# Performance work log

Measured on AMD Instinct MI355X. Metric: run time of the kernel, lower is better.

Reference implementation:

```python
import jax, jax.numpy as jnp
import numpy as np

EPS = 1e-5      # BatchNorm1d default eps
K = 4           # branching factor of the ontology tree
HID = 6         # num_hiddens_genotype
LEVEL_SIZES = (64, 16, 4, 1)   # leaves -> root (term_layer_list order)
OFFSETS = (0, 64, 80, 84)      # slices into the stacked [85,...] term params


def setup_inputs() -> dict:
    key = jax.random.key(0)
    ks = jax.random.split(key, 8)
    B, G, GD, NT, NL = 4096, 4096, 24, 85, 64
    f32 = jnp.float32
    return {
        "x": jax.random.normal(ks[0], (B, G), f32),
        "gene_W": jax.random.normal(ks[1], (NL, GD, G), f32) * (1.0 / np.sqrt(G)),
        "gene_b": jnp.zeros((NL, GD), f32),
        "term_W": jax.random.normal(ks[2], (NT, HID, GD), f32) * (1.0 / np.sqrt(GD)),
        "term_b": jnp.zeros((NT, HID), f32),
        "bn_gamma": jnp.ones((NT, HID), f32),
        "bn_beta": jnp.zeros((NT, HID), f32),
        "aux1_W": jax.random.normal(ks[3], (NT, 1, HID), f32) * 0.1,
        "aux1_b": jnp.zeros((NT, 1), f32),
        "aux2_W": jax.random.normal(ks[4], (NT, 1, 1), f32) * 0.1,
        "aux2_b": jnp.zeros((NT, 1), f32),
        "final_W": jax.random.normal(ks[5], (HID, HID), f32) * (1.0 / np.sqrt(HID)),
        "final_b": jnp.zeros((HID,), f32),
        "fbn_gamma": jnp.ones((HID,), f32),
        "fbn_beta": jnp.zeros((HID,), f32),
        "faux_W": jax.random.normal(ks[6], (1, HID), f32) * 0.1,
        "faux_b": jnp.zeros((1,), f32),
        "fout_W": jax.random.normal(ks[7], (1, 1), f32) * 0.1,
        "fout_b": jnp.zeros((1,), f32),
    }


def _bn(z, g, b):
    # training-mode BatchNorm1d: batch mean / biased variance over axis 0
    mu = jnp.mean(z, axis=0, keepdims=True)
    var = jnp.mean((z - mu) ** 2, axis=0, keepdims=True)
    return (z - mu) * jax.lax.rsqrt(var + EPS) * g + b


def _forward(x, gene_W, gene_b, term_W, term_b, bn_gamma, bn_beta,
             aux1_W, aux1_b, aux2_W, aux2_b, final_W, final_b,
             fbn_gamma, fbn_beta, faux_W, faux_b, fout_W, fout_b):
    B = x.shape[0]
    # direct_gene_layers for all 64 leaf terms, batched: [B, 64, 24]
    h_in = jnp.einsum('bg,tkg->btk', x, gene_W) + gene_b
    aux_outs = []
    h = None
    for n, o in zip(LEVEL_SIZES, OFFSETS):  # leaves -> root (DAG topo order)
        if h is not None:
            # concat the K=4 children hidden states of each term: [B,n,K*HID]
            h_in = h.reshape(B, n, K * HID)
        # per-term Linear + tanh + BatchNorm, batched over the n terms
        z = jnp.tanh(jnp.einsum('bti,thi->bth', h_in, term_W[o:o + n]) + term_b[o:o + n])
        h = _bn(z, bn_gamma[o:o + n], bn_beta[o:o + n])  # [B, n, HID]
        # aux head: Linear(HID->1) -> tanh -> Linear(1->1)
        a1 = jnp.tanh(jnp.einsum('bth,toh->bto', h, aux1_W[o:o + n]) + aux1_b[o:o + n])
        a2 = a1 * aux2_W[o:o + n, 0] + aux2_b[o:o + n]   # [B, n, 1]
        aux_outs.append(a2[..., 0])
    root = h[:, 0, :]                                    # [B, HID]
    f = jnp.tanh(root @ final_W.T + final_b)
    mu = jnp.mean(f, axis=0)
    var = jnp.mean((f - mu) ** 2, axis=0)
    f = (f - mu) * jax.lax.rsqrt(var + EPS) * fbn_gamma + fbn_beta
    fa = jnp.tanh(f @ faux_W.T + faux_b)                 # [B, 1]
    pred = jax.nn.sigmoid(fa * fout_W[0, 0] + fout_b)    # [B, 1]
    # aux_out_map flattened in topo order, with 'final' prediction last: [B, 86]
    return jnp.concatenate(aux_outs + [pred], axis=1)


def reference(x, gene_W, gene_b, term_W, term_b, bn_gamma, bn_beta,
              aux1_W, aux1_b, aux2_W, aux2_b, final_W, final_b,
              fbn_gamma, fbn_beta, faux_W, faux_b, fout_W, fout_b):
    return _forward(x, gene_W, gene_b, term_W, term_b, bn_gamma, bn_beta,
                    aux1_W, aux1_b, aux2_W, aux2_b, final_W, final_b,
                    fbn_gamma, fbn_beta, faux_W, faux_b, fout_W, fout_b)
```

## Files before the change

### kernel.cpp

```cpp
#include <hip/hip_runtime.h>
#include <stdint.h>
#include <math.h>

#define EPSV   1e-5f
#define BATCH  4096
#define GDIM   4096
#define NFEAT  1536

typedef __attribute__((ext_vector_type(8))) short bf16x8;
typedef __attribute__((ext_vector_type(4))) float f32x4;
typedef __attribute__((ext_vector_type(4))) uint32_t u32x4;

__device__ __forceinline__ uint32_t pkbf(float x, float y) {
    uint32_t a = __float_as_uint(x) + 0x8000u;
    uint32_t b = __float_as_uint(y) + 0x8000u;
    return __builtin_amdgcn_perm(b, a, 0x07060302u);
}
__device__ __forceinline__ uint16_t f2bf(float f) {
    return (uint16_t)((__float_as_uint(f) + 0x8000u) >> 16);
}
__device__ __forceinline__ void glds16(const uint16_t* g, short* l) {
    __builtin_amdgcn_global_load_lds(
        (const __attribute__((address_space(1))) void*)g,
        (__attribute__((address_space(3))) void*)l, 16, 0, 0);
}

__global__ __launch_bounds__(256) void cvt_bf16(
    const float* __restrict__ x, const float* __restrict__ w,
    uint16_t* __restrict__ xb, uint16_t* __restrict__ wb)
{
    const size_t NX = (size_t)BATCH * GDIM / 8;
    size_t i = (size_t)blockIdx.x * 256 + threadIdx.x;
    const float* src; uint16_t* dst;
    if (i < NX) { src = x + i * 8; dst = xb + i * 8; }
    else        { size_t j = i - NX; src = w + j * 8; dst = wb + j * 8; }
    f32x4 v0 = *(const f32x4*)src;
    f32x4 v1 = *(const f32x4*)(src + 4);
    u32x4 p = (u32x4){pkbf(v0[0],v0[1]), pkbf(v0[2],v0[3]),
                      pkbf(v1[0],v1[1]), pkbf(v1[2],v1[3])};
    *(u32x4*)dst = p;
}

__global__ __launch_bounds__(256) void gemm_glds(
    const uint16_t* __restrict__ A, const uint16_t* __restrict__ Bw,
    const float* __restrict__ bias, float* __restrict__ C0,
    uint16_t* __restrict__ C1, int KC)
{
    const int N = NFEAT, K = GDIM;
    __shared__ short sA[128 * 32];
    __shared__ short sB[128 * 32];
    const int tid  = threadIdx.x;
    const int m0   = blockIdx.y * 128, n0 = blockIdx.x * 128;
    const int kbase = blockIdx.z * KC;
    const int wave = tid >> 6, lane = tid & 63;
    const int wm   = (wave & 1) << 6, wn = (wave >> 1) << 6;
    const int lm   = lane & 15, quad = lane >> 4;

    f32x4 acc[4][4];
#pragma unroll
    for (int i = 0; i < 4; ++i)
#pragma unroll
        for (int j = 0; j < 4; ++j) acc[i][j] = (f32x4){0.f, 0.f, 0.f, 0.f};

    const int r0  = tid >> 2;
    const int c0e = (tid & 3) << 3;
    const uint16_t* gA = A  + (size_t)(m0 + r0) * K + kbase + c0e;
    const uint16_t* gB = Bw + (size_t)(n0 + r0) * K + kbase + c0e;
    short* la0 = &sA[tid * 8];
    short* la1 = &sA[2048 + tid * 8];
    short* lb0 = &sB[tid * 8];
    short* lb1 = &sB[2048 + tid * 8];
    const size_t rowskip = (size_t)64 * K;

    for (int k0 = 0; k0 < KC; k0 += 32) {
        __syncthreads();
        glds16(gA + k0,            la0);
        glds16(gA + rowskip + k0,  la1);
        glds16(gB + k0,            lb0);
        glds16(gB + rowskip + k0,  lb1);
        __syncthreads();
        bf16x8 af[4], bfr[4];
#pragma unroll
        for (int m = 0; m < 4; ++m)
            af[m]  = *(const bf16x8*)&sA[(wm + m * 16 + lm) * 32 + quad * 8];
#pragma unroll
        for (int n = 0; n < 4; ++n)
            bfr[n] = *(const bf16x8*)&sB[(wn + n * 16 + lm) * 32 + quad * 8];
#pragma unroll
        for (int m = 0; m < 4; ++m)
#pragma unroll
            for (int n = 0; n < 4; ++n)
                acc[m][n] = __builtin_amdgcn_mfma_f32_16x16x32_bf16(
                    af[m], bfr[n], acc[m][n], 0, 0, 0);
    }
    if (blockIdx.z == 0) {
#pragma unroll
        for (int n = 0; n < 4; ++n) {
            const int col = n0 + wn + n * 16 + lm;
            const float bv = bias[col];
#pragma unroll
            for (int m = 0; m < 4; ++m) {
                const int row = m0 + wm + m * 16 + (quad << 2);
                float* cp = C0 + (size_t)row * N + col;
#pragma unroll
                for (int r = 0; r < 4; ++r) cp[(size_t)r * N] = acc[m][n][r] + bv;
            }
        }
    } else {
#pragma unroll
        for (int n = 0; n < 4; ++n) {
            const int col = n0 + wn + n * 16 + lm;
#pragma unroll
            for (int m = 0; m < 4; ++m) {
                const int row = m0 + wm + m * 16 + (quad << 2);
                uint16_t* cp = C1 + (size_t)row * N + col;
#pragma unroll
                for (int r = 0; r < 4; ++r) cp[(size_t)r * N] = f2bf(acc[m][n][r]);
            }
        }
    }
}

__global__ __launch_bounds__(256) void gemm_bt(
    const float* __restrict__ A, const float* __restrict__ Bw,
    const float* __restrict__ bias, float* __restrict__ C, int KC)
{
    const int N = NFEAT, K = GDIM;
    __shared__ short sA[128 * 32];
    __shared__ short sB[128 * 32];
    const int tid  = threadIdx.x;
    const int m0   = blockIdx.y * 128, n0 = blockIdx.x * 128;
    const int kbase = blockIdx.z * KC;
    float* Cp = C + (size_t)blockIdx.z * ((size_t)BATCH * NFEAT);
    const int wave = tid >> 6, lane = tid & 63;
    const int wm   = (wave & 1) << 6, wn = (wave >> 1) << 6;
    const int lm   = lane & 15, quad = lane >> 4;

    f32x4 acc[4][4];
#pragma unroll
    for (int i = 0; i < 4; ++i)
#pragma unroll
        for (int j = 0; j < 4; ++j) acc[i][j] = (f32x4){0.f, 0.f, 0.f, 0.f};

    const int r0 = tid >> 2;
    const int c0 = (tid & 3) << 3;
    const float* ga = A  + (size_t)(m0 + r0) * K + kbase + c0;
    const float* gb = Bw + (size_t)(n0 + r0) * K + kbase + c0;
    uint32_t* wa = (uint32_t*)&sA[r0 * 32 + c0];
    uint32_t* wb = (uint32_t*)&sB[r0 * 32 + c0];
    const size_t rowskip = (size_t)64 * K;

    for (int k0 = 0; k0 < KC; k0 += 32) {
        f32x4 a00 = *(const f32x4*)(ga + k0);
        f32x4 a01 = *(const f32x4*)(ga + k0 + 4);
        f32x4 a10 = *(const f32x4*)(ga + rowskip + k0);
        f32x4 a11 = *(const f32x4*)(ga + rowskip + k0 + 4);
        f32x4 b00 = *(const f32x4*)(gb + k0);
        f32x4 b01 = *(const f32x4*)(gb + k0 + 4);
        f32x4 b10 = *(const f32x4*)(gb + rowskip + k0);
        f32x4 b11 = *(const f32x4*)(gb + rowskip + k0 + 4);
        u32x4 pa0 = (u32x4){pkbf(a00[0],a00[1]), pkbf(a00[2],a00[3]),
                            pkbf(a01[0],a01[1]), pkbf(a01[2],a01[3])};
        u32x4 pa1 = (u32x4){pkbf(a10[0],a10[1]), pkbf(a10[2],a10[3]),
                            pkbf(a11[0],a11[1]), pkbf(a11[2],a11[3])};
        u32x4 pb0 = (u32x4){pkbf(b00[0],b00[1]), pkbf(b00[2],b00[3]),
                            pkbf(b01[0],b01[1]), pkbf(b01[2],b01[3])};
        u32x4 pb1 = (u32x4){pkbf(b10[0],b10[1]), pkbf(b10[2],b10[3]),
                            pkbf(b11[0],b11[1]), pkbf(b11[2],b11[3])};
        __syncthreads();
        *(u32x4*)wa               = pa0;
        *(u32x4*)(wa + 64*32/2)   = pa1;
        *(u32x4*)wb               = pb0;
        *(u32x4*)(wb + 64*32/2)   = pb1;
        __syncthreads();
        bf16x8 af[4], bfr[4];
#pragma unroll
        for (int m = 0; m < 4; ++m)
            af[m]  = *(const bf16x8*)&sA[(wm + m * 16 + lm) * 32 + quad * 8];
#pragma unroll
        for (int n = 0; n < 4; ++n)
            bfr[n] = *(const bf16x8*)&sB[(wn + n * 16 + lm) * 32 + quad * 8];
#pragma unroll
        for (int m = 0; m < 4; ++m)
#pragma unroll
            for (int n = 0; n < 4; ++n)
                acc[m][n] = __builtin_amdgcn_mfma_f32_16x16x32_bf16(
                    af[m], bfr[n], acc[m][n], 0, 0, 0);
    }
#pragma unroll
    for (int n = 0; n < 4; ++n) {
        const int col = n0 + wn + n * 16 + lm;
        const float bv = (blockIdx.z == 0) ? bias[col] : 0.f;
#pragma unroll
        for (int m = 0; m < 4; ++m) {
            const int row = m0 + wm + m * 16 + (quad << 2);
            float* cp = Cp + (size_t)row * N + col;
#pragma unroll
            for (int r = 0; r < 4; ++r) cp[(size_t)r * N] = acc[m][n][r] + bv;
        }
    }
}

template <int N, int ROWS, bool HAS_PREV, int OFF, int PREV_OFF, int IN2MODE>
__global__ __launch_bounds__(256) void level_kernel(
    const float* __restrict__ in, const void* __restrict__ in2,
    float* __restrict__ z_out,
    const float* __restrict__ stats_prev, float* __restrict__ stats_out,
    const float* __restrict__ term_W, const float* __restrict__ term_b,
    const float* __restrict__ bn_gamma, const float* __restrict__ bn_beta,
    const float* __restrict__ aux1_W, const float* __restrict__ aux1_b,
    const float* __restrict__ aux2_W, const float* __restrict__ aux2_b,
    float* __restrict__ out)
{
    constexpr int IN_W  = 24 * N;
    constexpr int NF    = 6 * N;
    constexpr int NG    = 256 / N;
    constexpr int ITERS = (ROWS * N) / 256;
    constexpr int NPREV = HAS_PREV ? 4 * N : 1;

    __shared__ float Wl[144 * N];
    __shared__ float tbl[6 * N];
    __shared__ float aA[HAS_PREV ? IN_W : 1];
    __shared__ float aC[HAS_PREV ? IN_W : 1];
    __shared__ float a1wL[HAS_PREV ? 6 * NPREV : 1];
    __shared__ float a1bL[NPREV], a2wL[NPREV], a2bL[NPREV];
    __shared__ float ps[NG * NF], pq[NG * NF];

    const int tid = threadIdx.x;
    for (int idx = tid; idx < 144 * N; idx += 256) {
        int t = idx / 144, fh = idx - t * 144;
        Wl[fh * N + t] = term_W[(OFF + t) * 144 + fh];
    }
    for (int idx = tid; idx < 6 * N; idx += 256) {
        int t = idx / 6, h = idx - t * 6;
        tbl[h * N + t] = term_b[(OFF + t) * 6 + h];
    }
    if constexpr (HAS_PREV) {
        const float invB = 1.0f / BATCH;
        for (int j = tid; j < IN_W; j += 256) {
            float s = stats_prev[j], q = stats_prev[IN_W + j];
            float mu = s * invB;
            float var = q * invB - mu * mu;
            float rstd = rsqrtf(var + EPSV);
            float a = rstd * bn_gamma[PREV_OFF * 6 + j];
            int t = j / 24, i = j - t * 24;
            aA[i * N + t] = a;
            aC[i * N + t] = bn_beta[PREV_OFF * 6 + j] - mu * a;
        }
        for (int idx = tid; idx < 6 * NPREV; idx += 256) {
            int t = idx / 6, h = idx - t * 6;
            a1wL[h * NPREV + t] = aux1_W[(PREV_OFF + t) * 6 + h];
        }
        for (int t = tid; t < NPREV; t += 256) {
            a1bL[t] = aux1_b[PREV_OFF + t];
            a2wL[t] = aux2_W[PREV_OFF + t];
            a2bL[t] = aux2_b[PREV_OFF + t];
        }
    }
    __syncthreads();

    const int term = tid & (N - 1);
    const int grp  = tid / N;
    float s6[6], q6[6];
#pragma unroll
    for (int h = 0; h < 6; ++h) { s6[h] = 0.f; q6[h] = 0.f; }

    for (int it = 0; it < ITERS; ++it) {
        const int r = blockIdx.x * ROWS + it * NG + grp;
        const float* inrow = in + (size_t)r * IN_W + term * 24;
        float hv[24];
#pragma unroll
        for (int i4 = 0; i4 < 6; ++i4) {
            f32x4 v = *(const f32x4*)(inrow + 4 * i4);
            hv[4*i4+0] = v[0]; hv[4*i4+1] = v[1];
            hv[4*i4+2] = v[2]; hv[4*i4+3] = v[3];
        }
        if constexpr (IN2MODE == 1) {
            const float* inrow2 = (const float*)in2 + (size_t)r * IN_W + term * 24;
#pragma unroll
            for (int i4 = 0; i4 < 6; ++i4) {
                f32x4 v = *(const f32x4*)(inrow2 + 4 * i4);
                hv[4*i4+0] += v[0]; hv[4*i4+1] += v[1];
                hv[4*i4+2] += v[2]; hv[4*i4+3] += v[3];
            }
        } else if constexpr (IN2MODE == 2) {
            const uint32_t* p2 = (const uint32_t*)((const uint16_t*)in2 +
                                 (size_t)r * IN_W + term * 24);
#pragma unroll
            for (int i = 0; i < 12; ++i) {
                uint32_t u = p2[i];
                hv[2*i]   += __uint_as_float(u << 16);
                hv[2*i+1] += __uint_as_float(u & 0xffff0000u);
            }
        }
        if constexpr (HAS_PREV) {
#pragma unroll
            for (int i = 0; i < 24; ++i)
                hv[i] = hv[i] * aA[i * N + term] + aC[i * N + term];
#pragma unroll
            for (int s = 0; s < 4; ++s) {
                const int tp = term * 4 + s;
                float acc = a1bL[tp];
#pragma unroll
                for (int h2 = 0; h2 < 6; ++h2) acc += hv[s * 6 + h2] * a1wL[h2 * NPREV + tp];
                float a1 = tanhf(acc);
                out[(size_t)r * 86 + PREV_OFF + tp] = a1 * a2wL[tp] + a2bL[tp];
            }
        }
        float za[6];
#pragma unroll
        for (int h = 0; h < 6; ++h) za[h] = tbl[h * N + term];
#pragma unroll
        for (int i = 0; i < 24; ++i) {
            const float x = hv[i];
#pragma unroll
            for (int h = 0; h < 6; ++h) za[h] += x * Wl[(h * 24 + i) * N + term];
        }
        float* zr = z_out + (size_t)r * NF + term * 6;
#pragma unroll
        for (int h = 0; h < 6; ++h) {
            float z = tanhf(za[h]);
            zr[h] = z;
            s6[h] += z;
            q6[h] += z * z;
        }
    }
#pragma unroll
    for (int h = 0; h < 6; ++h) {
        ps[grp * NF + term * 6 + h] = s6[h];
        pq[grp * NF + term * 6 + h] = q6[h];
    }
    __syncthreads();
    for (int f = tid; f < NF; f += 256) {
        float s = 0.f, q = 0.f;
        for (int g2 = 0; g2 < NG; ++g2) { s += ps[g2 * NF + f]; q += pq[g2 * NF + f]; }
        atomicAdd(&stats_out[f], s);
        atomicAdd(&stats_out[NF + f], q);
    }
}

__global__ __launch_bounds__(1024) void final_fused(
    const float* __restrict__ z3, const float* __restrict__ st3,
    const float* __restrict__ bn_gamma, const float* __restrict__ bn_beta,
    const float* __restrict__ aux1_W, const float* __restrict__ aux1_b,
    const float* __restrict__ aux2_W, const float* __restrict__ aux2_b,
    const float* __restrict__ final_W, const float* __restrict__ final_b,
    const float* __restrict__ fbn_gamma, const float* __restrict__ fbn_beta,
    const float* __restrict__ faux_W, const float* __restrict__ faux_b,
    const float* __restrict__ fout_W, const float* __restrict__ fout_b,
    float* __restrict__ out)
{
    __shared__ float wred[16][12];
    __shared__ float fstat[12];
    const int tid = threadIdx.x;
    const float invB = 1.0f / BATCH;
    float a[6], c[6], fw[36], fbv[6];
#pragma unroll
    for (int j = 0; j < 6; ++j) {
        float s = st3[j], q = st3[6 + j];
        float mu = s * invB, var = q * invB - mu * mu;
        float rstd = rsqrtf(var + EPSV);
        a[j] = rstd * bn_gamma[84 * 6 + j];
        c[j] = bn_beta[84 * 6 + j] - mu * a[j];
        fbv[j] = final_b[j];
    }
#pragma unroll
    for (int j = 0; j < 36; ++j) fw[j] = final_W[j];

    float s6[6], q6[6];
#pragma unroll
    for (int j = 0; j < 6; ++j) { s6[j] = 0.f; q6[j] = 0.f; }

    for (int i = 0; i < 4; ++i) {
        const int r = i * 1024 + tid;
        float h[6];
#pragma unroll
        for (int j = 0; j < 6; ++j) h[j] = z3[(size_t)r * 6 + j] * a[j] + c[j];
        float acc = aux1_b[84];
#pragma unroll
        for (int j = 0; j < 6; ++j) acc += h[j] * aux1_W[84 * 6 + j];
        out[(size_t)r * 86 + 84] = tanhf(acc) * aux2_W[84] + aux2_b[84];
#pragma unroll
        for (int j = 0; j < 6; ++j) {
            float s = fbv[j];
#pragma unroll
            for (int k = 0; k < 6; ++k) s += h[k] * fw[j * 6 + k];
            float f = tanhf(s);
            s6[j] += f; q6[j] += f * f;
        }
    }
#pragma unroll
    for (int off = 32; off >= 1; off >>= 1) {
#pragma unroll
        for (int j = 0; j < 6; ++j) {
            s6[j] += __shfl_xor(s6[j], off, 64);
            q6[j] += __shfl_xor(q6[j], off, 64);
        }
    }
    const int wv = tid >> 6, ln = tid & 63;
    if (ln == 0) {
#pragma unroll
        for (int j = 0; j < 6; ++j) { wred[wv][j] = s6[j]; wred[wv][6 + j] = q6[j]; }
    }
    __syncthreads();
    if (tid < 12) {
        float s = 0.f;
#pragma unroll
        for (int w = 0; w < 16; ++w) s += wred[w][tid];
        fstat[tid] = s;
    }
    __syncthreads();
    float av[6], cv[6];
#pragma unroll
    for (int j = 0; j < 6; ++j) {
        float mu = fstat[j] * invB, var = fstat[6 + j] * invB - mu * mu;
        float rstd = rsqrtf(var + EPSV);
        av[j] = rstd * fbn_gamma[j];
        cv[j] = fbn_beta[j] - mu * av[j];
    }
    const float fxb0 = faux_b[0], foW0 = fout_W[0], fob0 = fout_b[0];
    for (int i = 0; i < 4; ++i) {
        const int r = i * 1024 + tid;
        float h[6];
#pragma unroll
        for (int j = 0; j < 6; ++j) h[j] = z3[(size_t)r * 6 + j] * a[j] + c[j];
        float acc2 = fxb0;
#pragma unroll
        for (int j = 0; j < 6; ++j) {
            float s = fbv[j];
#pragma unroll
            for (int k = 0; k < 6; ++k) s += h[k] * fw[j * 6 + k];
            float fn = tanhf(s) * av[j] + cv[j];
            acc2 += fn * faux_W[j];
        }
        float fa  = tanhf(acc2);
        float pre = fa * foW0 + fob0;
        out[(size_t)r * 86 + 85] = 1.0f / (1.0f + expf(-pre));
    }
}

extern "C" void kernel_launch(void* const* d_in, const int* in_sizes, int n_in,
                              void* d_out, int out_size, void* d_ws, size_t ws_size,
                              hipStream_t stream)
{
    const float* x      = (const float*)d_in[0];
    const float* gene_W = (const float*)d_in[1];
    const float* gene_b = (const float*)d_in[2];
    const float* term_W = (const float*)d_in[3];
    const float* term_b = (const float*)d_in[4];
    const float* bn_g   = (const float*)d_in[5];
    const float* bn_b   = (const float*)d_in[6];
    const float* a1W    = (const float*)d_in[7];
    const float* a1b    = (const float*)d_in[8];
    const float* a2W    = (const float*)d_in[9];
    const float* a2b    = (const float*)d_in[10];
    const float* fW     = (const float*)d_in[11];
    const float* fb     = (const float*)d_in[12];
    const float* fbn_g  = (const float*)d_in[13];
    const float* fbn_b  = (const float*)d_in[14];
    const float* fxW    = (const float*)d_in[15];
    const float* fxb    = (const float*)d_in[16];
    const float* foW    = (const float*)d_in[17];
    const float* fob    = (const float*)d_in[18];
    float* out = (float*)d_out;

    const size_t PART = 25165824;
    const size_t XB   = 33554432;
    const size_t WBS  = 12582912;
    const size_t P1B  = 12582912;
    const size_t TAILSZ = 6291456 + 1572864 + 393216 + 98304 + 4096;
    const size_t needA = XB + WBS + PART + P1B + TAILSZ;
    const size_t needB = 2 * PART + TAILSZ;
    const int plan = (ws_size >= needA) ? 0 : ((ws_size >= needB) ? 1 : 2);

    char* ws = (char*)d_ws;
    char* base;
    uint16_t *xbuf = nullptr, *wbuf = nullptr, *p1b = nullptr;
    float *p0, *p1f = nullptr;
    if (plan == 0) {
        xbuf = (uint16_t*)ws;
        wbuf = (uint16_t*)(ws + XB);
        p0   = (float*)(ws + XB + WBS);
        p1b  = (uint16_t*)(ws + XB + WBS + PART);
        base = ws + XB + WBS + PART + P1B;
    } else if (plan == 1) {
        p0   = (float*)ws;
        p1f  = (float*)(ws + PART);
        base = ws + 2 * PART;
    } else {
        p0   = (float*)ws;
        base = ws + PART;
    }
    float* z0 = (float*)(base);
    float* z1 = (float*)(base + 6291456);
    float* z2 = (float*)(base + 6291456 + 1572864);
    float* z3 = (float*)(base + 6291456 + 1572864 + 393216);
    float* stats = (float*)(base + 6291456 + 1572864 + 393216 + 98304);
    float* st0 = stats;
    float* st1 = stats + 768;
    float* st2 = stats + 960;
    float* st3 = stats + 1008;

    hipMemsetAsync(stats, 0, 1020 * sizeof(float), stream);
    if (plan == 0) {
        cvt_bf16<<<11264, 256, 0, stream>>>(x, gene_W, xbuf, wbuf);
        gemm_glds<<<dim3(12, 32, 2), 256, 0, stream>>>(xbuf, wbuf, gene_b, p0, p1b, GDIM / 2);
        level_kernel<64, 16, false, 0, 0, 2><<<256, 256, 0, stream>>>(
            p0, p1b, z0, nullptr, st0, term_W, term_b, bn_g, bn_b, a1W, a1b, a2W, a2b, out);
    } else if (plan == 1) {
        gemm_bt<<<dim3(12, 32, 2), 256, 0, stream>>>(x, gene_W, gene_b, p0, GDIM / 2);
        level_kernel<64, 16, false, 0, 0, 1><<<256, 256, 0, stream>>>(
            p0, p1f, z0, nullptr, st0, term_W, term_b, bn_g, bn_b, a1W, a1b, a2W, a2b, out);
    } else {
        gemm_bt<<<dim3(12, 32, 1), 256, 0, stream>>>(x, gene_W, gene_b, p0, GDIM);
        level_kernel<64, 16, false, 0, 0, 0><<<256, 256, 0, stream>>>(
            p0, nullptr, z0, nullptr, st0, term_W, term_b, bn_g, bn_b, a1W, a1b, a2W, a2b, out);
    }
    level_kernel<16, 16, true, 64, 0, 0><<<256, 256, 0, stream>>>(
        z0, nullptr, z1, st0, st1, term_W, term_b, bn_g, bn_b, a1W, a1b, a2W, a2b, out);
    level_kernel<4, 64, true, 80, 64, 0><<<64, 256, 0, stream>>>(
        z1, nullptr, z2, st1, st2, term_W, term_b, bn_g, bn_b, a1W, a1b, a2W, a2b, out);
    level_kernel<1, 256, true, 84, 80, 0><<<16, 256, 0, stream>>>(
        z2, nullptr, z3, st2, st3, term_W, term_b, bn_g, bn_b, a1W, a1b, a2W, a2b, out);
    final_fused<<<1, 1024, 0, stream>>>(
        z3, st3, bn_g, bn_b, a1W, a1b, a2W, a2b, fW, fb,
        fbn_g, fbn_b, fxW, fxb, foW, fob, out);
}
```

Baseline: 287.6 us.

## Fuse all tree levels and final head into one persistent kernel with grid barriers

Replaces the four per-level kernels and the final kernel with a single 256-block persistent kernel that keeps each block's 16 rows of intermediate activations in shared memory. BatchNorm batch statistics are accumulated with atomics and exchanged through software grid barriers between levels. The stats memset is folded into the bf16 conversion kernel, and the fallback fp32 GEMM plans are removed. This cuts launch overhead and global round-trips of the z buffers. The risks are deadlock if not all 256 blocks are co-resident, the cost of spinning at the barriers, and a hard dependency on the large workspace.

```diff
diff --git a/kernel.cpp b/kernel.cpp
--- a/kernel.cpp
+++ b/kernel.cpp
@@ -6,6 +6,7 @@
 #define BATCH  4096
 #define GDIM   4096
 #define NFEAT  1536
+#define NBLK   256
 
 typedef __attribute__((ext_vector_type(8))) short bf16x8;
 typedef __attribute__((ext_vector_type(4))) float f32x4;
@@ -24,11 +25,26 @@
         (const __attribute__((address_space(1))) void*)g,
         (__attribute__((address_space(3))) void*)l, 16, 0, 0);
 }
+__device__ __forceinline__ float aread(float* p) { return atomicAdd(p, 0.0f); }
+
+__device__ __forceinline__ void grid_barrier(int* bar, int target) {
+    __syncthreads();
+    if (threadIdx.x == 0) {
+        __threadfence();
+        atomicAdd(bar, 1);
+        while (__hip_atomic_load(bar, __ATOMIC_ACQUIRE, __HIP_MEMORY_SCOPE_AGENT) < target)
+            __builtin_amdgcn_s_sleep(2);
+    }
+    __syncthreads();
+}
 
 __global__ __launch_bounds__(256) void cvt_bf16(
     const float* __restrict__ x, const float* __restrict__ w,
-    uint16_t* __restrict__ xb, uint16_t* __restrict__ wb)
+    uint16_t* __restrict__ xb, uint16_t* __restrict__ wb,
+    float* __restrict__ stats)
 {
+    if (blockIdx.x == 0)
+        for (int j = threadIdx.x; j < 1040; j += 256) stats[j] = 0.f;
     const size_t NX = (size_t)BATCH * GDIM / 8;
     size_t i = (size_t)blockIdx.x * 256 + threadIdx.x;
     const float* src; uint16_t* dst;
@@ -121,321 +137,355 @@
     }
 }
 
-__global__ __launch_bounds__(256) void gemm_bt(
-    const float* __restrict__ A, const float* __restrict__ Bw,
-    const float* __restrict__ bias, float* __restrict__ C, int KC)
+__global__ __launch_bounds__(256) void tail_fused(
+    const float* __restrict__ p0, const uint16_t* __restrict__ p1b,
+    const float* __restrict__ term_W, const float* __restrict__ term_b,
+    const float* __restrict__ bn_g, const float* __restrict__ bn_b,
+    const float* __restrict__ a1W, const float* __restrict__ a1b,
+    const float* __restrict__ a2W, const float* __restrict__ a2b,
+    const float* __restrict__ fW, const float* __restrict__ fb,
+    const float* __restrict__ fbn_g, const float* __restrict__ fbn_b,
+    const float* __restrict__ fxW, const float* __restrict__ fxb,
+    const float* __restrict__ foW, const float* __restrict__ fob,
+    float* __restrict__ stats, float* __restrict__ out)
 {
-    const int N = NFEAT, K = GDIM;
-    __shared__ short sA[128 * 32];
-    __shared__ short sB[128 * 32];
-    const int tid  = threadIdx.x;
-    const int m0   = blockIdx.y * 128, n0 = blockIdx.x * 128;
-    const int kbase = blockIdx.z * KC;
-    float* Cp = C + (size_t)blockIdx.z * ((size_t)BATCH * NFEAT);
-    const int wave = tid >> 6, lane = tid & 63;
-    const int wm   = (wave & 1) << 6, wn = (wave >> 1) << 6;
-    const int lm   = lane & 15, quad = lane >> 4;
-
-    f32x4 acc[4][4];
-#pragma unroll
-    for (int i = 0; i < 4; ++i)
-#pragma unroll
-        for (int j = 0; j < 4; ++j) acc[i][j] = (f32x4){0.f, 0.f, 0.f, 0.f};
-
-    const int r0 = tid >> 2;
-    const int c0 = (tid & 3) << 3;
-    const float* ga = A  + (size_t)(m0 + r0) * K + kbase + c0;
-    const float* gb = Bw + (size_t)(n0 + r0) * K + kbase + c0;
-    uint32_t* wa = (uint32_t*)&sA[r0 * 32 + c0];
-    uint32_t* wb = (uint32_t*)&sB[r0 * 32 + c0];
-    const size_t rowskip = (size_t)64 * K;
-
-    for (int k0 = 0; k0 < KC; k0 += 32) {
-        f32x4 a00 = *(const f32x4*)(ga + k0);
-        f32x4 a01 = *(const f32x4*)(ga + k0 + 4);
-        f32x4 a10 = *(const f32x4*)(ga + rowskip + k0);
-        f32x4 a11 = *(const f32x4*)(ga + rowskip + k0 + 4);
-        f32x4 b00 = *(const f32x4*)(gb + k0);
-        f32x4 b01 = *(const f32x4*)(gb + k0 + 4);
-        f32x4 b10 = *(const f32x4*)(gb + rowskip + k0);
-        f32x4 b11 = *(const f32x4*)(gb + rowskip + k0 + 4);
-        u32x4 pa0 = (u32x4){pkbf(a00[0],a00[1]), pkbf(a00[2],a00[3]),
-                            pkbf(a01[0],a01[1]), pkbf(a01[2],a01[3])};
-        u32x4 pa1 = (u32x4){pkbf(a10[0],a10[1]), pkbf(a10[2],a10[3]),
-                            pkbf(a11[0],a11[1]), pkbf(a11[2],a11[3])};
-        u32x4 pb0 = (u32x4){pkbf(b00[0],b00[1]), pkbf(b00[2],b00[3]),
-                            pkbf(b01[0],b01[1]), pkbf(b01[2],b01[3])};
-        u32x4 pb1 = (u32x4){pkbf(b10[0],b10[1]), pkbf(b10[2],b10[3]),
-                            pkbf(b11[0],b11[1]), pkbf(b11[2],b11[3])};
-        __syncthreads();
-        *(u32x4*)wa               = pa0;
-        *(u32x4*)(wa + 64*32/2)   = pa1;
-        *(u32x4*)wb               = pb0;
-        *(u32x4*)(wb + 64*32/2)   = pb1;
-        __syncthreads();
-        bf16x8 af[4], bfr[4];
-#pragma unroll
-        for (int m = 0; m < 4; ++m)
-            af[m]  = *(const bf16x8*)&sA[(wm + m * 16 + lm) * 32 + quad * 8];
-#pragma unroll
-        for (int n = 0; n < 4; ++n)
-            bfr[n] = *(const bf16x8*)&sB[(wn + n * 16 + lm) * 32 + quad * 8];
-#pragma unroll
-        for (int m = 0; m < 4; ++m)
-#pragma unroll
-            for (int n = 0; n < 4; ++n)
-                acc[m][n] = __builtin_amdgcn_mfma_f32_16x16x32_bf16(
-                    af[m], bfr[n], acc[m][n], 0, 0, 0);
-    }
-#pragma unroll
-    for (int n = 0; n < 4; ++n) {
-        const int col = n0 + wn + n * 16 + lm;
-        const float bv = (blockIdx.z == 0) ? bias[col] : 0.f;
-#pragma unroll
-        for (int m = 0; m < 4; ++m) {
-            const int row = m0 + wm + m * 16 + (quad << 2);
-            float* cp = Cp + (size_t)row * N + col;
-#pragma unroll
-            for (int r = 0; r < 4; ++r) cp[(size_t)r * N] = acc[m][n][r] + bv;
-        }
-    }
-}
-
-template <int N, int ROWS, bool HAS_PREV, int OFF, int PREV_OFF, int IN2MODE>
-__global__ __launch_bounds__(256) void level_kernel(
-    const float* __restrict__ in, const void* __restrict__ in2,
-    float* __restrict__ z_out,
-    const float* __restrict__ stats_prev, float* __restrict__ stats_out,
-    const float* __restrict__ term_W, const float* __restrict__ term_b,
-    const float* __restrict__ bn_gamma, const float* __restrict__ bn_beta,
-    const float* __restrict__ aux1_W, const float* __restrict__ aux1_b,
-    const float* __restrict__ aux2_W, const float* __restrict__ aux2_b,
-    float* __restrict__ out)
-{
-    constexpr int IN_W  = 24 * N;
-    constexpr int NF    = 6 * N;
-    constexpr int NG    = 256 / N;
-    constexpr int ITERS = (ROWS * N) / 256;
-    constexpr int NPREV = HAS_PREV ? 4 * N : 1;
-
-    __shared__ float Wl[144 * N];
-    __shared__ float tbl[6 * N];
-    __shared__ float aA[HAS_PREV ? IN_W : 1];
-    __shared__ float aC[HAS_PREV ? IN_W : 1];
-    __shared__ float a1wL[HAS_PREV ? 6 * NPREV : 1];
-    __shared__ float a1bL[NPREV], a2wL[NPREV], a2bL[NPREV];
-    __shared__ float ps[NG * NF], pq[NG * NF];
+    float* st0 = stats;
+    float* st1 = stats + 768;
+    float* st2 = stats + 960;
+    float* st3 = stats + 1008;
+    float* fst = stats + 1020;
+    int*   bar = (int*)(stats + 1032);
+
+    __shared__ float Wl0[144 * 64], tbl0[6 * 64];
+    __shared__ float Wl1[144 * 16], tbl1[6 * 16];
+    __shared__ float Wl2[144 * 4],  tbl2[6 * 4];
+    __shared__ float Wl3[144],      tbl3[6];
+    __shared__ float z0L[16 * 385];
+    __shared__ float z1L[16 * 97];
+    __shared__ float z2L[16 * 25];
+    __shared__ float z3L[16 * 7];
+    __shared__ float fL [16 * 6];
+    __shared__ float aAb[384], aCb[384];
+    __shared__ float a1wb[384], a1bb[64], a2wb[64], a2bb[64];
+    __shared__ float ps[1536], pq[1536];
+    __shared__ float r12[12], a3L[6], c3L[6], avL[6], cvL[6];
 
     const int tid = threadIdx.x;
-    for (int idx = tid; idx < 144 * N; idx += 256) {
+    const int rbase = blockIdx.x * 16;
+    const float invB = 1.0f / BATCH;
+
+    for (int idx = tid; idx < 144 * 64; idx += 256) {
         int t = idx / 144, fh = idx - t * 144;
-        Wl[fh * N + t] = term_W[(OFF + t) * 144 + fh];
-    }
-    for (int idx = tid; idx < 6 * N; idx += 256) {
+        Wl0[fh * 64 + t] = term_W[t * 144 + fh];
+    }
+    for (int idx = tid; idx < 144 * 16; idx += 256) {
+        int t = idx / 144, fh = idx - t * 144;
+        Wl1[fh * 16 + t] = term_W[(64 + t) * 144 + fh];
+    }
+    for (int idx = tid; idx < 144 * 4; idx += 256) {
+        int t = idx / 144, fh = idx - t * 144;
+        Wl2[fh * 4 + t] = term_W[(80 + t) * 144 + fh];
+    }
+    for (int idx = tid; idx < 144; idx += 256) Wl3[idx] = term_W[84 * 144 + idx];
+    for (int idx = tid; idx < 384; idx += 256) {
         int t = idx / 6, h = idx - t * 6;
-        tbl[h * N + t] = term_b[(OFF + t) * 6 + h];
-    }
-    if constexpr (HAS_PREV) {
-        const float invB = 1.0f / BATCH;
-        for (int j = tid; j < IN_W; j += 256) {
-            float s = stats_prev[j], q = stats_prev[IN_W + j];
-            float mu = s * invB;
-            float var = q * invB - mu * mu;
-            float rstd = rsqrtf(var + EPSV);
-            float a = rstd * bn_gamma[PREV_OFF * 6 + j];
-            int t = j / 24, i = j - t * 24;
-            aA[i * N + t] = a;
-            aC[i * N + t] = bn_beta[PREV_OFF * 6 + j] - mu * a;
-        }
-        for (int idx = tid; idx < 6 * NPREV; idx += 256) {
-            int t = idx / 6, h = idx - t * 6;
-            a1wL[h * NPREV + t] = aux1_W[(PREV_OFF + t) * 6 + h];
-        }
-        for (int t = tid; t < NPREV; t += 256) {
-            a1bL[t] = aux1_b[PREV_OFF + t];
-            a2wL[t] = aux2_W[PREV_OFF + t];
-            a2bL[t] = aux2_b[PREV_OFF + t];
-        }
-    }
+        tbl0[h * 64 + t] = term_b[t * 6 + h];
+    }
+    for (int idx = tid; idx < 96; idx += 256) {
+        int t = idx / 6, h = idx - t * 6;
+        tbl1[h * 16 + t] = term_b[(64 + t) * 6 + h];
+    }
+    if (tid < 24) { int t = tid / 6, h = tid - t * 6; tbl2[h * 4 + t] = term_b[(80 + t) * 6 + h]; }
+    if (tid < 6)  tbl3[tid] = term_b[84 * 6 + tid];
     __syncthreads();
 
-    const int term = tid & (N - 1);
-    const int grp  = tid / N;
-    float s6[6], q6[6];
-#pragma unroll
-    for (int h = 0; h < 6; ++h) { s6[h] = 0.f; q6[h] = 0.f; }
-
-    for (int it = 0; it < ITERS; ++it) {
-        const int r = blockIdx.x * ROWS + it * NG + grp;
-        const float* inrow = in + (size_t)r * IN_W + term * 24;
-        float hv[24];
-#pragma unroll
-        for (int i4 = 0; i4 < 6; ++i4) {
-            f32x4 v = *(const f32x4*)(inrow + 4 * i4);
-            hv[4*i4+0] = v[0]; hv[4*i4+1] = v[1];
-            hv[4*i4+2] = v[2]; hv[4*i4+3] = v[3];
-        }
-        if constexpr (IN2MODE == 1) {
-            const float* inrow2 = (const float*)in2 + (size_t)r * IN_W + term * 24;
+    {
+        const int term = tid & 63, grp = tid >> 6;
+        float s6[6], q6[6];
+#pragma unroll
+        for (int h = 0; h < 6; ++h) { s6[h] = 0.f; q6[h] = 0.f; }
+        for (int it = 0; it < 4; ++it) {
+            const int rl = it * 4 + grp;
+            const int r  = rbase + rl;
+            const float* inrow = p0 + (size_t)r * NFEAT + term * 24;
+            float hv[24];
 #pragma unroll
             for (int i4 = 0; i4 < 6; ++i4) {
-                f32x4 v = *(const f32x4*)(inrow2 + 4 * i4);
-                hv[4*i4+0] += v[0]; hv[4*i4+1] += v[1];
-                hv[4*i4+2] += v[2]; hv[4*i4+3] += v[3];
-            }
-        } else if constexpr (IN2MODE == 2) {
-            const uint32_t* p2 = (const uint32_t*)((const uint16_t*)in2 +
-                                 (size_t)r * IN_W + term * 24);
+                f32x4 v = *(const f32x4*)(inrow + 4 * i4);
+                hv[4*i4+0] = v[0]; hv[4*i4+1] = v[1];
+                hv[4*i4+2] = v[2]; hv[4*i4+3] = v[3];
+            }
+            const uint32_t* p2 = (const uint32_t*)(p1b + (size_t)r * NFEAT + term * 24);
 #pragma unroll
             for (int i = 0; i < 12; ++i) {
                 uint32_t u = p2[i];
                 hv[2*i]   += __uint_as_float(u << 16);
                 hv[2*i+1] += __uint_as_float(u & 0xffff0000u);
             }
-        }
-        if constexpr (HAS_PREV) {
+            float za[6];
+#pragma unroll
+            for (int h = 0; h < 6; ++h) za[h] = tbl0[h * 64 + term];
+#pragma unroll
+            for (int i = 0; i < 24; ++i) {
+                const float xv = hv[i];
+#pragma unroll
+                for (int h = 0; h < 6; ++h) za[h] += xv * Wl0[(h * 24 + i) * 64 + term];
+            }
+#pragma unroll
+            for (int h = 0; h < 6; ++h) {
+                float z = tanhf(za[h]);
+                z0L[rl * 385 + term * 6 + h] = z;
+                s6[h] += z; q6[h] += z * z;
+            }
+        }
+#pragma unroll
+        for (int h = 0; h < 6; ++h) {
+            ps[grp * 384 + term * 6 + h] = s6[h];
+            pq[grp * 384 + term * 6 + h] = q6[h];
+        }
+        __syncthreads();
+        for (int f = tid; f < 384; f += 256) {
+            float s = 0.f, q = 0.f;
+#pragma unroll
+            for (int g = 0; g < 4; ++g) { s += ps[g * 384 + f]; q += pq[g * 384 + f]; }
+            atomicAdd(&st0[f], s);
+            atomicAdd(&st0[384 + f], q);
+        }
+    }
+    grid_barrier(bar, NBLK * 1);
+
+    {
+        for (int j = tid; j < 384; j += 256) {
+            float s = aread(&st0[j]), q = aread(&st0[384 + j]);
+            float mu = s * invB, var = q * invB - mu * mu;
+            float a = rsqrtf(var + EPSV) * bn_g[j];
+            int t = j / 24, i = j - t * 24;
+            aAb[i * 16 + t] = a;
+            aCb[i * 16 + t] = bn_b[j] - mu * a;
+        }
+        for (int idx = tid; idx < 384; idx += 256) {
+            int t = idx / 6, h = idx - t * 6;
+            a1wb[h * 64 + t] = a1W[t * 6 + h];
+        }
+        if (tid < 64) { a1bb[tid] = a1b[tid]; a2wb[tid] = a2W[tid]; a2bb[tid] = a2b[tid]; }
+        __syncthreads();
+
+        const int term = tid & 15, grp = tid >> 4;
+        const int r = rbase + grp;
+        float hv[24];
+#pragma unroll
+        for (int i = 0; i < 24; ++i)
+            hv[i] = z0L[grp * 385 + term * 24 + i] * aAb[i * 16 + term] + aCb[i * 16 + term];
+#pragma unroll
+        for (int s = 0; s < 4; ++s) {
+            const int tp = term * 4 + s;
+            float acc = a1bb[tp];
+#pragma unroll
+            for (int h2 = 0; h2 < 6; ++h2) acc += hv[s * 6 + h2] * a1wb[h2 * 64 + tp];
+            out[(size_t)r * 86 + tp] = tanhf(acc) * a2wb[tp] + a2bb[tp];
+        }
+        float za[6];
+#pragma unroll
+        for (int h = 0; h < 6; ++h) za[h] = tbl1[h * 16 + term];
+#pragma unroll
+        for (int i = 0; i < 24; ++i) {
+            const float xv = hv[i];
+#pragma unroll
+            for (int h = 0; h < 6; ++h) za[h] += xv * Wl1[(h * 24 + i) * 16 + term];
+        }
+#pragma unroll
+        for (int h = 0; h < 6; ++h) {
+            float z = tanhf(za[h]);
+            z1L[grp * 97 + term * 6 + h] = z;
+            ps[grp * 96 + term * 6 + h] = z;
+            pq[grp * 96 + term * 6 + h] = z * z;
+        }
+        __syncthreads();
+        for (int f = tid; f < 96; f += 256) {
+            float s = 0.f, q = 0.f;
+#pragma unroll
+            for (int g = 0; g < 16; ++g) { s += ps[g * 96 + f]; q += pq[g * 96 + f]; }
+            atomicAdd(&st1[f], s);
+            atomicAdd(&st1[96 + f], q);
+        }
+    }
+    grid_barrier(bar, NBLK * 2);
+
+    {
+        for (int j = tid; j < 96; j += 256) {
+            float s = aread(&st1[j]), q = aread(&st1[96 + j]);
+            float mu = s * invB, var = q * invB - mu * mu;
+            float a = rsqrtf(var + EPSV) * bn_g[64 * 6 + j];
+            int t = j / 24, i = j - t * 24;
+            aAb[i * 4 + t] = a;
+            aCb[i * 4 + t] = bn_b[64 * 6 + j] - mu * a;
+        }
+        for (int idx = tid; idx < 96; idx += 256) {
+            int t = idx / 6, h = idx - t * 6;
+            a1wb[h * 16 + t] = a1W[(64 + t) * 6 + h];
+        }
+        if (tid < 16) { a1bb[tid] = a1b[64 + tid]; a2wb[tid] = a2W[64 + tid]; a2bb[tid] = a2b[64 + tid]; }
+        __syncthreads();
+
+        const int term = tid & 3, row = tid >> 2;
+        if (row < 16) {
+            const int r = rbase + row;
+            float hv[24];
 #pragma unroll
             for (int i = 0; i < 24; ++i)
-                hv[i] = hv[i] * aA[i * N + term] + aC[i * N + term];
+                hv[i] = z1L[row * 97 + term * 24 + i] * aAb[i * 4 + term] + aCb[i * 4 + term];
 #pragma unroll
             for (int s = 0; s < 4; ++s) {
                 const int tp = term * 4 + s;
-                float acc = a1bL[tp];
-#pragma unroll
-                for (int h2 = 0; h2 < 6; ++h2) acc += hv[s * 6 + h2] * a1wL[h2 * NPREV + tp];
-                float a1 = tanhf(acc);
-                out[(size_t)r * 86 + PREV_OFF + tp] = a1 * a2wL[tp] + a2bL[tp];
-            }
-        }
-        float za[6];
-#pragma unroll
-        for (int h = 0; h < 6; ++h) za[h] = tbl[h * N + term];
-#pragma unroll
-        for (int i = 0; i < 24; ++i) {
-            const float x = hv[i];
-#pragma unroll
-            for (int h = 0; h < 6; ++h) za[h] += x * Wl[(h * 24 + i) * N + term];
-        }
-        float* zr = z_out + (size_t)r * NF + term * 6;
-#pragma unroll
-        for (int h = 0; h < 6; ++h) {
-            float z = tanhf(za[h]);
-            zr[h] = z;
-            s6[h] += z;
-            q6[h] += z * z;
-        }
-    }
-#pragma unroll
-    for (int h = 0; h < 6; ++h) {
-        ps[grp * NF + term * 6 + h] = s6[h];
-        pq[grp * NF + term * 6 + h] = q6[h];
-    }
-    __syncthreads();
-    for (int f = tid; f < NF; f += 256) {
-        float s = 0.f, q = 0.f;
-        for (int g2 = 0; g2 < NG; ++g2) { s += ps[g2 * NF + f]; q += pq[g2 * NF + f]; }
-        atomicAdd(&stats_out[f], s);
-        atomicAdd(&stats_out[NF + f], q);
-    }
-}
-
-__global__ __launch_bounds__(1024) void final_fused(
-    const float* __restrict__ z3, const float* __restrict__ st3,
-    const float* __restrict__ bn_gamma, const float* __restrict__ bn_beta,
-    const float* __restrict__ aux1_W, const float* __restrict__ aux1_b,
-    const float* __restrict__ aux2_W, const float* __restrict__ aux2_b,
-    const float* __restrict__ final_W, const float* __restrict__ final_b,
-    const float* __restrict__ fbn_gamma, const float* __restrict__ fbn_beta,
-    const float* __restrict__ faux_W, const float* __restrict__ faux_b,
-    const float* __restrict__ fout_W, const float* __restrict__ fout_b,
-    float* __restrict__ out)
-{
-    __shared__ float wred[16][12];
-    __shared__ float fstat[12];
-    const int tid = threadIdx.x;
-    const float invB = 1.0f / BATCH;
-    float a[6], c[6], fw[36], fbv[6];
-#pragma unroll
-    for (int j = 0; j < 6; ++j) {
-        float s = st3[j], q = st3[6 + j];
-        float mu = s * invB, var = q * invB - mu * mu;
-        float rstd = rsqrtf(var + EPSV);
-        a[j] = rstd * bn_gamma[84 * 6 + j];
-        c[j] = bn_beta[84 * 6 + j] - mu * a[j];
-        fbv[j] = final_b[j];
-    }
-#pragma unroll
-    for (int j = 0; j < 36; ++j) fw[j] = final_W[j];
-
-    float s6[6], q6[6];
-#pragma unroll
-    for (int j = 0; j < 6; ++j) { s6[j] = 0.f; q6[j] = 0.f; }
-
-    for (int i = 0; i < 4; ++i) {
-        const int r = i * 1024 + tid;
-        float h[6];
-#pragma unroll
-        for (int j = 0; j < 6; ++j) h[j] = z3[(size_t)r * 6 + j] * a[j] + c[j];
-        float acc = aux1_b[84];
-#pragma unroll
-        for (int j = 0; j < 6; ++j) acc += h[j] * aux1_W[84 * 6 + j];
-        out[(size_t)r * 86 + 84] = tanhf(acc) * aux2_W[84] + aux2_b[84];
-#pragma unroll
-        for (int j = 0; j < 6; ++j) {
-            float s = fbv[j];
-#pragma unroll
-            for (int k = 0; k < 6; ++k) s += h[k] * fw[j * 6 + k];
-            float f = tanhf(s);
-            s6[j] += f; q6[j] += f * f;
-        }
-    }
-#pragma unroll
-    for (int off = 32; off >= 1; off >>= 1) {
-#pragma unroll
-        for (int j = 0; j < 6; ++j) {
-            s6[j] += __shfl_xor(s6[j], off, 64);
-            q6[j] += __shfl_xor(q6[j], off, 64);
-        }
-    }
-    const int wv = tid >> 6, ln = tid & 63;
-    if (ln == 0) {
-#pragma unroll
-        for (int j = 0; j < 6; ++j) { wred[wv][j] = s6[j]; wred[wv][6 + j] = q6[j]; }
-    }
-    __syncthreads();
-    if (tid < 12) {
-        float s = 0.f;
-#pragma unroll
-        for (int w = 0; w < 16; ++w) s += wred[w][tid];
-        fstat[tid] = s;
-    }
-    __syncthreads();
-    float av[6], cv[6];
-#pragma unroll
-    for (int j = 0; j < 6; ++j) {
-        float mu = fstat[j] * invB, var = fstat[6 + j] * invB - mu * mu;
-        float rstd = rsqrtf(var + EPSV);
-        av[j] = rstd * fbn_gamma[j];
-        cv[j] = fbn_beta[j] - mu * av[j];
-    }
-    const float fxb0 = faux_b[0], foW0 = fout_W[0], fob0 = fout_b[0];
-    for (int i = 0; i < 4; ++i) {
-        const int r = i * 1024 + tid;
-        float h[6];
-#pragma unroll
-        for (int j = 0; j < 6; ++j) h[j] = z3[(size_t)r * 6 + j] * a[j] + c[j];
-        float acc2 = fxb0;
-#pragma unroll
-        for (int j = 0; j < 6; ++j) {
-            float s = fbv[j];
-#pragma unroll
-            for (int k = 0; k < 6; ++k) s += h[k] * fw[j * 6 + k];
-            float fn = tanhf(s) * av[j] + cv[j];
-            acc2 += fn * faux_W[j];
-        }
-        float fa  = tanhf(acc2);
-        float pre = fa * foW0 + fob0;
-        out[(size_t)r * 86 + 85] = 1.0f / (1.0f + expf(-pre));
+                float acc = a1bb[tp];
+#pragma unroll
+                for (int h2 = 0; h2 < 6; ++h2) acc += hv[s * 6 + h2] * a1wb[h2 * 16 + tp];
+                out[(size_t)r * 86 + 64 + tp] = tanhf(acc) * a2wb[tp] + a2bb[tp];
+            }
+            float za[6];
+#pragma unroll
+            for (int h = 0; h < 6; ++h) za[h] = tbl2[h * 4 + term];
+#pragma unroll
+            for (int i = 0; i < 24; ++i) {
+                const float xv = hv[i];
+#pragma unroll
+                for (int h = 0; h < 6; ++h) za[h] += xv * Wl2[(h * 24 + i) * 4 + term];
+            }
+#pragma unroll
+            for (int h = 0; h < 6; ++h) {
+                float z = tanhf(za[h]);
+                z2L[row * 25 + term * 6 + h] = z;
+                ps[row * 24 + term * 6 + h] = z;
+                pq[row * 24 + term * 6 + h] = z * z;
+            }
+        }
+        __syncthreads();
+        if (tid < 24) {
+            float s = 0.f, q = 0.f;
+#pragma unroll
+            for (int g = 0; g < 16; ++g) { s += ps[g * 24 + tid]; q += pq[g * 24 + tid]; }
+            atomicAdd(&st2[tid], s);
+            atomicAdd(&st2[24 + tid], q);
+        }
+    }
+    grid_barrier(bar, NBLK * 3);
+
+    {
+        if (tid < 24) {
+            float s = aread(&st2[tid]), q = aread(&st2[24 + tid]);
+            float mu = s * invB, var = q * invB - mu * mu;
+            float a = rsqrtf(var + EPSV) * bn_g[80 * 6 + tid];
+            aAb[tid] = a;
+            aCb[tid] = bn_b[80 * 6 + tid] - mu * a;
+        }
+        if (tid < 24) { int t = tid / 6, h = tid - t * 6; a1wb[h * 4 + t] = a1W[(80 + t) * 6 + h]; }
+        if (tid < 4) { a1bb[tid] = a1b[80 + tid]; a2wb[tid] = a2W[80 + tid]; a2bb[tid] = a2b[80 + tid]; }
+        __syncthreads();
+
+        const int row = tid;
+        if (row < 16) {
+            const int r = rbase + row;
+            float hv[24];
+#pragma unroll
+            for (int i = 0; i < 24; ++i)
+                hv[i] = z2L[row * 25 + i] * aAb[i] + aCb[i];
+#pragma unroll
+            for (int s = 0; s < 4; ++s) {
+                float acc = a1bb[s];
+#pragma unroll
+                for (int h2 = 0; h2 < 6; ++h2) acc += hv[s * 6 + h2] * a1wb[h2 * 4 + s];
+                out[(size_t)r * 86 + 80 + s] = tanhf(acc) * a2wb[s] + a2bb[s];
+            }
+            float za[6];
+#pragma unroll
+            for (int h = 0; h < 6; ++h) za[h] = tbl3[h];
+#pragma unroll
+            for (int i = 0; i < 24; ++i) {
+                const float xv = hv[i];
+#pragma unroll
+                for (int h = 0; h < 6; ++h) za[h] += xv * Wl3[h * 24 + i];
+            }
+#pragma unroll
+            for (int h = 0; h < 6; ++h) {
+                float z = tanhf(za[h]);
+                z3L[row * 7 + h] = z;
+                ps[row * 6 + h] = z;
+                pq[row * 6 + h] = z * z;
+            }
+        }
+        __syncthreads();
+        if (tid < 6) {
+            float s = 0.f, q = 0.f;
+#pragma unroll
+            for (int g = 0; g < 16; ++g) { s += ps[g * 6 + tid]; q += pq[g * 6 + tid]; }
+            atomicAdd(&st3[tid], s);
+            atomicAdd(&st3[6 + tid], q);
+        }
+    }
+    grid_barrier(bar, NBLK * 4);
+
+    {
+        if (tid < 12) r12[tid] = aread(&st3[tid]);
+        __syncthreads();
+        if (tid < 6) {
+            float mu = r12[tid] * invB, var = r12[6 + tid] * invB - mu * mu;
+            float a = rsqrtf(var + EPSV) * bn_g[84 * 6 + tid];
+            a3L[tid] = a;
+            c3L[tid] = bn_b[84 * 6 + tid] - mu * a;
+        }
+        __syncthreads();
+        const int row = tid;
+        if (row < 16) {
+            const int r = rbase + row;
+            float h[6];
+#pragma unroll
+            for (int j = 0; j < 6; ++j) h[j] = z3L[row * 7 + j] * a3L[j] + c3L[j];
+            float acc = a1b[84];
+#pragma unroll
+            for (int j = 0; j < 6; ++j) acc += h[j] * a1W[84 * 6 + j];
+            out[(size_t)r * 86 + 84] = tanhf(acc) * a2W[84] + a2b[84];
+#pragma unroll
+            for (int j = 0; j < 6; ++j) {
+                float s = fb[j];
+#pragma unroll
+                for (int k = 0; k < 6; ++k) s += h[k] * fW[j * 6 + k];
+                float f = tanhf(s);
+                fL[row * 6 + j] = f;
+                ps[row * 6 + j] = f;
+                pq[row * 6 + j] = f * f;
+            }
+        }
+        __syncthreads();
+        if (tid < 6) {
+            float s = 0.f, q = 0.f;
+#pragma unroll
+            for (int g = 0; g < 16; ++g) { s += ps[g * 6 + tid]; q += pq[g * 6 + tid]; }
+            atomicAdd(&fst[tid], s);
+            atomicAdd(&fst[6 + tid], q);
+        }
+    }
+    grid_barrier(bar, NBLK * 5);
+
+    {
+        if (tid < 12) r12[tid] = aread(&fst[tid]);
+        __syncthreads();
+        if (tid < 6) {
+            float mu = r12[tid] * invB, var = r12[6 + tid] * invB - mu * mu;
+            float a = rsqrtf(var + EPSV) * fbn_g[tid];
+            avL[tid] = a;
+            cvL[tid] = fbn_b[tid] - mu * a;
+        }
+        __syncthreads();
+        const int row = tid;
+        if (row < 16) {
+            const int r = rbase + row;
+            float acc = fxb[0];
+#pragma unroll
+            for (int j = 0; j < 6; ++j)
+                acc += (fL[row * 6 + j] * avL[j] + cvL[j]) * fxW[j];
+            float pre = tanhf(acc) * foW[0] + fob[0];
+            out[(size_t)r * 86 + 85] = 1.0f / (1.0f + expf(-pre));
+        }
     }
 }
 
@@ -464,65 +514,21 @@
     const float* fob    = (const float*)d_in[18];
     float* out = (float*)d_out;
 
-    const size_t PART = 25165824;
-    const size_t XB   = 33554432;
-    const size_t WBS  = 12582912;
-    const size_t P1B  = 12582912;
-    const size_t TAILSZ = 6291456 + 1572864 + 393216 + 98304 + 4096;
-    const size_t needA = XB + WBS + PART + P1B + TAILSZ;
-    const size_t needB = 2 * PART + TAILSZ;
-    const int plan = (ws_size >= needA) ? 0 : ((ws_size >= needB) ? 1 : 2);
+    const size_t XB  = 33554432;
+    const size_t WBS = 12582912;
+    const size_t P0  = 25165824;
+    const size_t P1B = 12582912;
 
     char* ws = (char*)d_ws;
-    char* base;
-    uint16_t *xbuf = nullptr, *wbuf = nullptr, *p1b = nullptr;
-    float *p0, *p1f = nullptr;
-    if (plan == 0) {
-        xbuf = (uint16_t*)ws;
-        wbuf = (uint16_t*)(ws + XB);
-        p0   = (float*)(ws + XB + WBS);
-        p1b  = (uint16_t*)(ws + XB + WBS + PART);
-        base = ws + XB + WBS + PART + P1B;
-    } else if (plan == 1) {
-        p0   = (float*)ws;
-        p1f  = (float*)(ws + PART);
-        base = ws + 2 * PART;
-    } else {
-        p0   = (float*)ws;
-        base = ws + PART;
-    }
-    float* z0 = (float*)(base);
-    float* z1 = (float*)(base + 6291456);
-    float* z2 = (float*)(base + 6291456 + 1572864);
-    float* z3 = (float*)(base + 6291456 + 1572864 + 393216);
-    float* stats = (float*)(base + 6291456 + 1572864 + 393216 + 98304);
-    float* st0 = stats;
-    float* st1 = stats + 768;
-    float* st2 = stats + 960;
-    float* st3 = stats + 1008;
-
-    hipMemsetAsync(stats, 0, 1020 * sizeof(float), stream);
-    if (plan == 0) {
-        cvt_bf16<<<11264, 256, 0, stream>>>(x, gene_W, xbuf, wbuf);
-        gemm_glds<<<dim3(12, 32, 2), 256, 0, stream>>>(xbuf, wbuf, gene_b, p0, p1b, GDIM / 2);
-        level_kernel<64, 16, false, 0, 0, 2><<<256, 256, 0, stream>>>(
-            p0, p1b, z0, nullptr, st0, term_W, term_b, bn_g, bn_b, a1W, a1b, a2W, a2b, out);
-    } else if (plan == 1) {
-        gemm_bt<<<dim3(12, 32, 2), 256, 0, stream>>>(x, gene_W, gene_b, p0, GDIM / 2);
-        level_kernel<64, 16, false, 0, 0, 1><<<256, 256, 0, stream>>>(
-            p0, p1f, z0, nullptr, st0, term_W, term_b, bn_g, bn_b, a1W, a1b, a2W, a2b, out);
-    } else {
-        gemm_bt<<<dim3(12, 32, 1), 256, 0, stream>>>(x, gene_W, gene_b, p0, GDIM);
-        level_kernel<64, 16, false, 0, 0, 0><<<256, 256, 0, stream>>>(
-            p0, nullptr, z0, nullptr, st0, term_W, term_b, bn_g, bn_b, a1W, a1b, a2W, a2b, out);
-    }
-    level_kernel<16, 16, true, 64, 0, 0><<<256, 256, 0, stream>>>(
-        z0, nullptr, z1, st0, st1, term_W, term_b, bn_g, bn_b, a1W, a1b, a2W, a2b, out);
-    level_kernel<4, 64, true, 80, 64, 0><<<64, 256, 0, stream>>>(
-        z1, nullptr, z2, st1, st2, term_W, term_b, bn_g, bn_b, a1W, a1b, a2W, a2b, out);
-    level_kernel<1, 256, true, 84, 80, 0><<<16, 256, 0, stream>>>(
-        z2, nullptr, z3, st2, st3, term_W, term_b, bn_g, bn_b, a1W, a1b, a2W, a2b, out);
-    final_fused<<<1, 1024, 0, stream>>>(
-        z3, st3, bn_g, bn_b, a1W, a1b, a2W, a2b, fW, fb,
-        fbn_g, fbn_b, fxW, fxb, foW, fob, out);
-}
+    uint16_t* xbuf = (uint16_t*)ws;
+    uint16_t* wbuf = (uint16_t*)(ws + XB);
+    float*    p0   = (float*)(ws + XB + WBS);
+    uint16_t* p1b  = (uint16_t*)(ws + XB + WBS + P0);
+    float*    stats = (float*)(ws + XB + WBS + P0 + P1B);
+
+    cvt_bf16<<<11264, 256, 0, stream>>>(x, gene_W, xbuf, wbuf, stats);
+    gemm_glds<<<dim3(12, 32, 2), 256, 0, stream>>>(xbuf, wbuf, gene_b, p0, p1b, GDIM / 2);
+    tail_fused<<<NBLK, 256, 0, stream>>>(
+        p0, p1b, term_W, term_b, bn_g, bn_b, a1W, a1b, a2W, a2b,
+        fW, fb, fbn_g, fbn_b, fxW, fxb, foW, fob, stats, out);
+}
```

Measured after the change: 341.1 us. 18.6% more time.
